# Kernel optimization log

Measured on AMD Instinct MI355X. Metric: run time of the kernel, lower is better.

Reference implementation:

```python
import jax, jax.numpy as jnp
import numpy as np

N, C, H, W = 64, 160, 64, 64
DIM, M = 160, 6
N_ITERS = 2
EPS_LN = 1e-5


def layer_norm(x, g, b):
    mu = jnp.mean(x, axis=-1, keepdims=True)
    var = jnp.var(x, axis=-1, keepdims=True)
    return (x - mu) * jax.lax.rsqrt(var + EPS_LN) * g + b


def setup_inputs() -> dict:
    key = jax.random.key(0)
    ks = jax.random.split(key, 10)
    d = DIM
    lin = lambda k, i, o: jax.random.normal(k, (i, o), jnp.float32) * (1.0 / np.sqrt(i))
    return {
        "feat": jax.random.normal(ks[0], (N, C, H, W), jnp.float32),
        "slots_init": jax.random.normal(ks[1], (M, d), jnp.float32) * 0.02,
        "log_tau": jnp.zeros((1,), jnp.float32),
        "kv_g": jnp.ones((C,), jnp.float32), "kv_b": jnp.zeros((C,), jnp.float32),
        "Wk": lin(ks[2], C, d), "Wv": lin(ks[3], C, d),
        "q_g": jnp.ones((d,), jnp.float32), "q_b": jnp.zeros((d,), jnp.float32),
        "Wq": lin(ks[4], d, d),
        "out_g": jnp.ones((d,), jnp.float32), "out_b": jnp.zeros((d,), jnp.float32),
        "W1": lin(ks[5], d, 2 * d), "b1": jnp.zeros((2 * d,), jnp.float32),
        "W2": lin(ks[6], 2 * d, d), "b2": jnp.zeros((d,), jnp.float32),
    }


def reference(feat, slots_init, log_tau, kv_g, kv_b, Wk, Wv, q_g, q_b, Wq,
              out_g, out_b, W1, b1, W2, b2):
    n, c, h, w = feat.shape
    scale = DIM ** (-0.5)
    # [n, l, c] tokens
    kv_in = layer_norm(feat.reshape(n, c, h * w).transpose(0, 2, 1), kv_g, kv_b)
    k = kv_in @ Wk  # [n, l, d]
    v = kv_in @ Wv  # [n, l, d]
    slots = jnp.broadcast_to(slots_init[None], (n, M, DIM))
    tau = jax.nn.softplus(log_tau) + 0.5  # [1]
    attn = None
    for _ in range(N_ITERS):
        q = layer_norm(slots, q_g, q_b) @ Wq  # [n, m, d]
        logits = jnp.einsum('nmd,nld->nml', q, k) * (scale / tau)
        attn = jax.nn.softmax(logits, axis=1)  # compete over slots
        weights = attn / jnp.clip(attn.sum(axis=-1, keepdims=True), 1e-6)
        updates = jnp.einsum('nml,nld->nmd', weights, v)
        slots = layer_norm(slots + updates, out_g, out_b)
        slots = slots + (jax.nn.gelu(slots @ W1 + b1, approximate=False) @ W2 + b2)
    attn_map = (attn / jnp.clip(attn.sum(axis=-1, keepdims=True), 1e-6)).reshape(n, M, h, w)
    return slots, attn_map
```

## Files before the change

### kernel.cpp

```cpp
#include <hip/hip_runtime.h>
#include <math.h>

#define NN 64
#define CC 160
#define LL 4096
#define DD 160
#define MM 6
#define NCH 64
#define XSTR 68
#define PSPL 8

#if defined(__has_builtin)
#if __has_builtin(__builtin_amdgcn_fdot2_f32_bf16)
#define HAVE_DOT2 1
#endif
#endif

__device__ __forceinline__ unsigned short f2bf(float f) {
  union { float f; unsigned int i; } v; v.f = f;
  unsigned int r = v.i + 0x7fffu + ((v.i >> 16) & 1u);
  return (unsigned short)(r >> 16);
}
__device__ __forceinline__ float u2f_lo(unsigned int w) {
  union { unsigned int i; float f; } v; v.i = w << 16; return v.f;
}
__device__ __forceinline__ float u2f_hi(unsigned int w) {
  union { unsigned int i; float f; } v; v.i = w & 0xffff0000u; return v.f;
}

#if HAVE_DOT2
typedef __bf16 v2bf __attribute__((ext_vector_type(2)));
__device__ __forceinline__ float dot2bf(unsigned int a, unsigned int b, float c) {
  union { unsigned int u; v2bf v; } ua, ub;
  ua.u = a; ub.u = b;
  return __builtin_amdgcn_fdot2_f32_bf16(ua.v, ub.v, c, false);
}
#else
__device__ __forceinline__ float dot2bf(unsigned int a, unsigned int b, float c) {
  return fmaf(u2f_hi(a), u2f_hi(b), fmaf(u2f_lo(a), u2f_lo(b), c));
}
#endif

__global__ __launch_bounds__(256) void k_init(
    const float* log_tau, const float* slots_init, const float* q_g, const float* q_b,
    const float* Wq, const float* Wk, float* Wkq1, float* scal) {
  __shared__ float ln[MM * DD];
  __shared__ float qv[MM * DD];
  __shared__ float mu_s[MM], rs_s[MM];
  int tid = threadIdx.x;
  float x = log_tau[0];
  float sp = (x > 20.f) ? x : log1pf(expf(x));
  float scv = (1.0f / sqrtf((float)DD)) / (sp + 0.5f);
  if (blockIdx.x == 0 && tid == 0) scal[0] = scv;
  if (tid < MM) {
    float s = 0.f, ss = 0.f;
    for (int i = 0; i < DD; i++) { float v = slots_init[tid * DD + i]; s += v; ss += v * v; }
    float mu = s / DD, var = ss / DD - mu * mu;
    mu_s[tid] = mu; rs_s[tid] = rsqrtf(var + 1e-5f);
  }
  __syncthreads();
  for (int o = tid; o < MM * DD; o += 256) {
    int m = o / DD, d = o % DD;
    ln[o] = (slots_init[o] - mu_s[m]) * rs_s[m] * q_g[d] + q_b[d];
  }
  __syncthreads();
  for (int o = tid; o < MM * DD; o += 256) {
    int m = o / DD, d = o % DD;
    float acc = 0.f;
#pragma unroll 8
    for (int i = 0; i < DD; i++) acc += ln[m * DD + i] * Wq[i * DD + d];
    qv[o] = acc;
  }
  __syncthreads();
  for (int o = tid; o < 60; o += 256) {
    int c = blockIdx.x * 10 + o / 6, m = o % 6;
    float acc = 0.f;
#pragma unroll 8
    for (int d = 0; d < DD; d++) acc += Wk[c * DD + d] * qv[m * DD + d];
    Wkq1[c * 6 + m] = scv * acc;
  }
}

__global__ __launch_bounds__(256) void k_init2(
    const float* Wkq1, const float* kv_g, const float* kv_b, float* P1, float* ab) {
  int tid = threadIdx.x;
  for (int o = tid; o < DD * 6; o += 256) {
    int c = o / 6;
    P1[o] = kv_g[c] * Wkq1[o];
  }
  if (tid < 192) {
    int grp = tid >> 4;
    int l = tid & 15;
    int m = grp % 6;
    const float* coef = (grp < 6) ? kv_g : kv_b;
    float s = 0.f;
#pragma unroll
    for (int i = 0; i < 10; i++) {
      int c = l + i * 16;
      s += coef[c] * Wkq1[c * 6 + m];
    }
    s += __shfl_xor(s, 1); s += __shfl_xor(s, 2);
    s += __shfl_xor(s, 4); s += __shfl_xor(s, 8);
    if (l == 0) ab[grp] = s;
  }
}

template <bool ITER2>
__global__ __launch_bounds__(256) void k_pass(
    const float* __restrict__ feat, const float* __restrict__ Pg,
    const float* __restrict__ abg, float* __restrict__ Apart,
    float* __restrict__ SWpart, float* __restrict__ attn_out) {
  int b = blockIdx.x;
  int n = b >> 6, ch = b & 63;
  int tid = threadIdx.x;
  int lane = tid & 63, g = tid >> 6;
  int cg = lane >> 4, tl = lane & 15;

  __shared__ __align__(16) unsigned short xb[160 * XSTR];
  __shared__ __align__(8) float part[4][16][4][10];
  __shared__ __align__(16) unsigned int w2_s[32][8];
  __shared__ __align__(16) float P_s[160][8];

  const float* wsrc = ITER2 ? (Pg + (size_t)n * DD * 6) : Pg;
  for (int o = tid; o < DD * 6; o += 256) P_s[o / 6][o % 6] = wsrc[o];
  const float* absrc = ITER2 ? (abg + n * 12) : abg;
  float alpha[6], beta[6];
#pragma unroll
  for (int m = 0; m < 6; m++) { alpha[m] = absrc[m]; beta[m] = absrc[6 + m]; }
  __syncthreads();

  const float* fb = feat + ((size_t)(n * CC + g * 40 + cg)) * LL + ch * 64 + 4 * tl;
  float s4[4] = {0, 0, 0, 0}, ss4[4] = {0, 0, 0, 0};
  float lgr[6][4];
#pragma unroll
  for (int m = 0; m < 6; m++) { lgr[m][0] = 0.f; lgr[m][1] = 0.f; lgr[m][2] = 0.f; lgr[m][3] = 0.f; }
#pragma unroll
  for (int r = 0; r < 10; r++) {
    int c = g * 40 + r * 4 + cg;
    float4 xv = *(const float4*)(fb + (size_t)(r * 4) * LL);
    float4 p03 = *(const float4*)&P_s[c][0];
    float2 p45 = *(const float2*)&P_s[c][4];
    float xs[4] = {xv.x, xv.y, xv.z, xv.w};
#pragma unroll
    for (int j = 0; j < 4; j++) {
      float x = xs[j];
      s4[j] += x; ss4[j] = fmaf(x, x, ss4[j]);
      lgr[0][j] = fmaf(x, p03.x, lgr[0][j]); lgr[1][j] = fmaf(x, p03.y, lgr[1][j]);
      lgr[2][j] = fmaf(x, p03.z, lgr[2][j]); lgr[3][j] = fmaf(x, p03.w, lgr[3][j]);
      lgr[4][j] = fmaf(x, p45.x, lgr[4][j]); lgr[5][j] = fmaf(x, p45.y, lgr[5][j]);
    }
    uint2 pk;
    pk.x = (unsigned int)f2bf(xv.x) | ((unsigned int)f2bf(xv.y) << 16);
    pk.y = (unsigned int)f2bf(xv.z) | ((unsigned int)f2bf(xv.w) << 16);
    *(uint2*)&xb[c * XSTR + 4 * tl] = pk;
  }
#pragma unroll
  for (int j = 0; j < 4; j++) {
    s4[j] += __shfl_xor(s4[j], 16);  s4[j] += __shfl_xor(s4[j], 32);
    ss4[j] += __shfl_xor(ss4[j], 16); ss4[j] += __shfl_xor(ss4[j], 32);
#pragma unroll
    for (int m = 0; m < 6; m++) {
      lgr[m][j] += __shfl_xor(lgr[m][j], 16);
      lgr[m][j] += __shfl_xor(lgr[m][j], 32);
    }
  }
  if (cg == 0) {
#pragma unroll
    for (int j = 0; j < 4; j++) {
      float* pp = &part[g][tl][j][0];
      *(float2*)&pp[0] = make_float2(s4[j], ss4[j]);
      *(float2*)&pp[2] = make_float2(lgr[0][j], lgr[1][j]);
      *(float2*)&pp[4] = make_float2(lgr[2][j], lgr[3][j]);
      *(float2*)&pp[6] = make_float2(lgr[4][j], lgr[5][j]);
    }
  }
  __syncthreads();

  {
    int tg = lane >> 2, tj = lane & 3;
    float S = 0.f, SS = 0.f, L[6] = {0, 0, 0, 0, 0, 0};
#pragma unroll
    for (int g2 = 0; g2 < 4; g2++) {
      const float* pp = &part[g2][tg][tj][0];
      float2 a = *(const float2*)&pp[0];
      float2 b2_ = *(const float2*)&pp[2];
      float2 c2 = *(const float2*)&pp[4];
      float2 d2 = *(const float2*)&pp[6];
      S += a.x; SS += a.y;
      L[0] += b2_.x; L[1] += b2_.y; L[2] += c2.x; L[3] += c2.y; L[4] += d2.x; L[5] += d2.y;
    }
    float mu = S * (1.0f / CC);
    float var = SS * (1.0f / CC) - mu * mu;
    float rs = rsqrtf(var + 1e-5f);
    float lg[6];
#pragma unroll
    for (int m = 0; m < 6; m++) lg[m] = rs * L[m] - rs * mu * alpha[m] + beta[m];
    float mx = lg[0];
#pragma unroll
    for (int m = 1; m < 6; m++) mx = fmaxf(mx, lg[m]);
    float e[6], sum = 0.f;
#pragma unroll
    for (int m = 0; m < 6; m++) { e[m] = __expf(lg[m] - mx); sum += e[m]; }
    float inv = 1.0f / sum;
    float att[6], wv[6];
#pragma unroll
    for (int m = 0; m < 6; m++) { att[m] = e[m] * inv; wv[m] = att[m] * rs; }

    if (g == 0) {
      float wo[6];
#pragma unroll
      for (int m = 0; m < 6; m++) wo[m] = __shfl_xor(wv[m], 1);
      if (!(lane & 1)) {
        int tp = lane >> 1;
        unsigned int pk[6];
#pragma unroll
        for (int m = 0; m < 6; m++) pk[m] = (unsigned int)f2bf(wv[m]) | ((unsigned int)f2bf(wo[m]) << 16);
        *(uint4*)&w2_s[tp][0] = make_uint4(pk[0], pk[1], pk[2], pk[3]);
        *(uint2*)&w2_s[tp][4] = make_uint2(pk[4], pk[5]);
      }
    } else if (g == 1) {
      if (ITER2) {
        size_t ob = ((size_t)(n * MM)) * LL + ch * 64 + lane;
#pragma unroll
        for (int m = 0; m < 6; m++) attn_out[ob + (size_t)m * LL] = att[m];
      }
    } else if (g == 2) {
#pragma unroll
      for (int m = 0; m < 6; m++) {
        float v = att[m];
        v += __shfl_xor(v, 1);  v += __shfl_xor(v, 2);  v += __shfl_xor(v, 4);
        v += __shfl_xor(v, 8);  v += __shfl_xor(v, 16); v += __shfl_xor(v, 32);
        if (lane == 0) SWpart[b * 12 + m] = v;
      }
    } else {
#pragma unroll
      for (int m = 0; m < 6; m++) {
        float v = wv[m] * mu;
        v += __shfl_xor(v, 1);  v += __shfl_xor(v, 2);  v += __shfl_xor(v, 4);
        v += __shfl_xor(v, 8);  v += __shfl_xor(v, 16); v += __shfl_xor(v, 32);
        if (lane == 0) SWpart[b * 12 + 6 + m] = v;
      }
    }
  }
  __syncthreads();

  if (tid < DD) {
    float A0 = 0.f, A1 = 0.f, A2 = 0.f, A3 = 0.f, A4 = 0.f, A5 = 0.f;
    const unsigned short* xr = &xb[tid * XSTR];
#pragma unroll
    for (int k = 0; k < 16; k++) {
      uint2 xw = *(const uint2*)(xr + 4 * k);
      uint4 wa0 = *(const uint4*)&w2_s[2 * k][0];
      uint2 wb0 = *(const uint2*)&w2_s[2 * k][4];
      uint4 wa1 = *(const uint4*)&w2_s[2 * k + 1][0];
      uint2 wb1 = *(const uint2*)&w2_s[2 * k + 1][4];
      A0 = dot2bf(wa0.x, xw.x, A0); A1 = dot2bf(wa0.y, xw.x, A1);
      A2 = dot2bf(wa0.z, xw.x, A2); A3 = dot2bf(wa0.w, xw.x, A3);
      A4 = dot2bf(wb0.x, xw.x, A4); A5 = dot2bf(wb0.y, xw.x, A5);
      A0 = dot2bf(wa1.x, xw.y, A0); A1 = dot2bf(wa1.y, xw.y, A1);
      A2 = dot2bf(wa1.z, xw.y, A2); A3 = dot2bf(wa1.w, xw.y, A3);
      A4 = dot2bf(wb1.x, xw.y, A4); A5 = dot2bf(wb1.y, xw.y, A5);
    }
    float Aacc[6] = {A0, A1, A2, A3, A4, A5};
#pragma unroll
    for (int m = 0; m < 6; m++) Apart[((size_t)b * 6 + m) * DD + tid] = Aacc[m];
  }
}

__global__ __launch_bounds__(256) void k_reduce(
    const float* __restrict__ Apart, const float* __restrict__ SWpart,
    float* __restrict__ Ared8, float* __restrict__ SWred8) {
  int b = blockIdx.x;
  int n = b / 48;
  int r = b % 48;
  int m = r >> 3, ps = r & 7;
  int tid = threadIdx.x;
  if (tid < DD) {
    const float* src = Apart + ((size_t)(n * NCH + ps * 8) * 6 + m) * DD + tid;
    float s0 = src[0 * 6 * DD] + src[1 * 6 * DD];
    float s1 = src[2 * 6 * DD] + src[3 * 6 * DD];
    float s2 = src[4 * 6 * DD] + src[5 * 6 * DD];
    float s3 = src[6 * 6 * DD] + src[7 * 6 * DD];
    Ared8[((size_t)(n * PSPL + ps) * 6 + m) * DD + tid] = (s0 + s1) + (s2 + s3);
  } else if (m == 0 && tid >= 192 && tid < 204) {
    int k = tid - 192;
    const float* src = SWpart + (size_t)(n * NCH + ps * 8) * 12 + k;
    float s0 = src[0 * 12] + src[1 * 12];
    float s1 = src[2 * 12] + src[3 * 12];
    float s2 = src[4 * 12] + src[5 * 12];
    float s3 = src[6 * 12] + src[7 * 12];
    SWred8[(n * PSPL + ps) * 12 + k] = (s0 + s1) + (s2 + s3);
  }
}

template <bool FIRST, bool LAST>
__global__ __launch_bounds__(256) void k_slot3(
    const float* __restrict__ slots_init, const float* __restrict__ Ared8,
    const float* __restrict__ SWred8, const float* __restrict__ Wv,
    const float* __restrict__ out_g, const float* __restrict__ out_b,
    const float* __restrict__ W1, const float* __restrict__ b1,
    const float* __restrict__ W2, const float* __restrict__ b2,
    const float* __restrict__ q_g, const float* __restrict__ q_b,
    const float* __restrict__ Wq, const float* __restrict__ Wk,
    const float* __restrict__ kv_g, const float* __restrict__ kv_b,
    const float* __restrict__ scal,
    float* __restrict__ slotbuf, float* __restrict__ P2, float* __restrict__ ab2,
    float* __restrict__ Sfin, float* __restrict__ out_slots) {
  int b = blockIdx.x;
  int n = b / MM, m = b % MM;
  int tid = threadIdx.x;
  __shared__ float a_s[DD];
  __shared__ float s1[DD];
  __shared__ float h[320];
  __shared__ float pg[DD], pb[DD];
  __shared__ float sw_s[2];
  __shared__ float Sv_s, mu_s, rs_s;

  if (tid < 16) {
    int ps = tid & 7, which = tid >> 3;
    float v = SWred8[(size_t)(n * PSPL + ps) * 12 + m + 6 * which];
    v += __shfl_xor(v, 1); v += __shfl_xor(v, 2); v += __shfl_xor(v, 4);
    if (ps == 0) {
      if (which == 0) {
        sw_s[0] = v;
        float sc = fmaxf(v, 1e-6f);
        Sv_s = sc;
        if (LAST) Sfin[n * 6 + m] = sc;
      } else {
        sw_s[1] = v;
      }
    }
  }
  __syncthreads();
  if (tid < DD) {
    const float* src = Ared8 + ((size_t)(n * PSPL) * 6 + m) * DD + tid;
    float ar = 0.f;
#pragma unroll
    for (int ps = 0; ps < PSPL; ps++) ar += src[(size_t)ps * 6 * DD];
    a_s[tid] = kv_g[tid] * (ar - sw_s[1]) + kv_b[tid] * sw_s[0];
  }
  __syncthreads();
  if (tid < DD) {
    float u = 0.f;
#pragma unroll 8
    for (int c = 0; c < DD; c++) u = fmaf(a_s[c], Wv[c * DD + tid], u);
    float prev = FIRST ? slots_init[m * DD + tid] : slotbuf[(size_t)n * MM * DD + m * DD + tid];
    s1[tid] = prev + u / Sv_s;
  }
  __syncthreads();
  if (tid < 64) {
    float x0 = s1[tid], x1 = s1[tid + 64], x2 = (tid < 32) ? s1[tid + 128] : 0.f;
    float s = x0 + x1 + x2, ss = x0 * x0 + x1 * x1 + x2 * x2;
#pragma unroll
    for (int off = 32; off >= 1; off >>= 1) { s += __shfl_xor(s, off); ss += __shfl_xor(ss, off); }
    if (tid == 0) {
      float mu = s / DD, var = ss / DD - mu * mu;
      mu_s = mu; rs_s = rsqrtf(var + 1e-5f);
    }
  }
  __syncthreads();
  if (tid < DD) s1[tid] = (s1[tid] - mu_s) * rs_s * out_g[tid] + out_b[tid];
  __syncthreads();
  for (int j = tid; j < 320; j += 256) {
    float acc = b1[j];
#pragma unroll 8
    for (int d = 0; d < DD; d++) acc = fmaf(s1[d], W1[d * 320 + j], acc);
    h[j] = 0.5f * acc * (1.0f + erff(acc * 0.70710678118f));
  }
  __syncthreads();
  if (tid < DD) {
    float acc = b2[tid];
#pragma unroll 8
    for (int j = 0; j < 320; j++) acc = fmaf(h[j], W2[j * DD + tid], acc);
    float val = s1[tid] + acc;
    a_s[tid] = val;
    if (LAST) out_slots[(size_t)n * MM * DD + m * DD + tid] = val;
    else slotbuf[(size_t)n * MM * DD + m * DD + tid] = val;
  }
  if (!LAST) {
    __syncthreads();
    if (tid < 64) {
      float x0 = a_s[tid], x1 = a_s[tid + 64], x2 = (tid < 32) ? a_s[tid + 128] : 0.f;
      float s = x0 + x1 + x2, ss = x0 * x0 + x1 * x1 + x2 * x2;
#pragma unroll
      for (int off = 32; off >= 1; off >>= 1) { s += __shfl_xor(s, off); ss += __shfl_xor(ss, off); }
      if (tid == 0) {
        float mu = s / DD, var = ss / DD - mu * mu;
        mu_s = mu; rs_s = rsqrtf(var + 1e-5f);
      }
    }
    __syncthreads();
    if (tid < DD) s1[tid] = (a_s[tid] - mu_s) * rs_s * q_g[tid] + q_b[tid];
    __syncthreads();
    if (tid < DD) {
      float acc = 0.f;
#pragma unroll 8
      for (int i = 0; i < DD; i++) acc = fmaf(s1[i], Wq[i * DD + tid], acc);
      h[tid] = acc;
    }
    __syncthreads();
    {
      int grp = tid >> 4, l = tid & 15;
      float sc = scal[0];
#pragma unroll 2
      for (int p = 0; p < 10; p++) {
        int c = p * 16 + grp;
        float s = 0.f;
#pragma unroll
        for (int i = 0; i < 10; i++) {
          int d = l + i * 16;
          s = fmaf(Wk[c * DD + d], h[d], s);
        }
        s += __shfl_xor(s, 1); s += __shfl_xor(s, 2);
        s += __shfl_xor(s, 4); s += __shfl_xor(s, 8);
        if (l == 0) {
          float wr = sc * s;
          float gv = kv_g[c] * wr;
          P2[(size_t)n * DD * 6 + c * 6 + m] = gv;
          pg[c] = gv;
          pb[c] = kv_b[c] * wr;
        }
      }
    }
    __syncthreads();
    if (tid < 128) {
      int w = tid >> 6, l = tid & 63;
      const float* src = (w == 0) ? pg : pb;
      float x0 = src[l], x1 = src[l + 64], x2 = (l < 32) ? src[l + 128] : 0.f;
      float s = x0 + x1 + x2;
#pragma unroll
      for (int off = 32; off >= 1; off >>= 1) s += __shfl_xor(s, off);
      if (l == 0) ab2[n * 12 + 6 * w + m] = s;
    }
  }
}

__global__ __launch_bounds__(256) void k_norm(float* attn, const float* Sfin) {
  int idx = blockIdx.x * 256 + threadIdx.x;
  size_t base = (size_t)idx * 4;
  int nm = (int)(base >> 12);
  float s = Sfin[nm];
  float4 v = *(float4*)(attn + base);
  float inv = 1.0f / s;
  v.x *= inv; v.y *= inv; v.z *= inv; v.w *= inv;
  *(float4*)(attn + base) = v;
}

extern "C" void kernel_launch(void* const* d_in, const int* in_sizes, int n_in,
                              void* d_out, int out_size, void* d_ws, size_t ws_size,
                              hipStream_t stream) {
  const float* feat       = (const float*)d_in[0];
  const float* slots_init = (const float*)d_in[1];
  const float* log_tau    = (const float*)d_in[2];
  const float* kv_g       = (const float*)d_in[3];
  const float* kv_b       = (const float*)d_in[4];
  const float* Wk         = (const float*)d_in[5];
  const float* Wv         = (const float*)d_in[6];
  const float* q_g        = (const float*)d_in[7];
  const float* q_b        = (const float*)d_in[8];
  const float* Wq         = (const float*)d_in[9];
  const float* out_g      = (const float*)d_in[10];
  const float* out_b      = (const float*)d_in[11];
  const float* W1         = (const float*)d_in[12];
  const float* b1         = (const float*)d_in[13];
  const float* W2         = (const float*)d_in[14];
  const float* b2         = (const float*)d_in[15];
  float* out = (float*)d_out;
  float* out_attn = out + NN * MM * DD;

  float* Wkq1   = (float*)d_ws;
  float* ab     = Wkq1 + DD * 6;
  float* P1     = ab + 16;
  float* P2     = P1 + DD * 6;
  float* ab2    = P2 + (size_t)NN * DD * 6;
  float* Apart  = ab2 + NN * 12;
  float* SWpart = Apart + (size_t)NN * NCH * MM * DD;
  float* Ared8  = SWpart + (size_t)NN * NCH * 12;
  float* SWred8 = Ared8 + (size_t)NN * PSPL * MM * DD;
  float* Sfin   = SWred8 + NN * PSPL * 12;
  float* scal   = Sfin + NN * MM;
  float* slotbuf = scal + 8;
  size_t required = (size_t)((char*)(slotbuf + NN * MM * DD) - (char*)d_ws);
  if (ws_size < required) return;

  k_init<<<16, 256, 0, stream>>>(log_tau, slots_init, q_g, q_b, Wq, Wk, Wkq1, scal);
  k_init2<<<1, 256, 0, stream>>>(Wkq1, kv_g, kv_b, P1, ab);
  k_pass<false><<<NN * NCH, 256, 0, stream>>>(feat, P1, ab, Apart, SWpart, out_attn);
  k_reduce<<<NN * MM * PSPL, 256, 0, stream>>>(Apart, SWpart, Ared8, SWred8);
  k_slot3<true, false><<<NN * MM, 256, 0, stream>>>(slots_init, Ared8, SWred8, Wv, out_g, out_b,
                                                    W1, b1, W2, b2, q_g, q_b, Wq, Wk, kv_g, kv_b, scal,
                                                    slotbuf, P2, ab2, Sfin, out);
  k_pass<true><<<NN * NCH, 256, 0, stream>>>(feat, P2, ab2, Apart, SWpart, out_attn);
  k_reduce<<<NN * MM * PSPL, 256, 0, stream>>>(Apart, SWpart, Ared8, SWred8);
  k_slot3<false, true><<<NN * MM, 256, 0, stream>>>(slots_init, Ared8, SWred8, Wv, out_g, out_b,
                                                    W1, b1, W2, b2, q_g, q_b, Wq, Wk, kv_g, kv_b, scal,
                                                    slotbuf, P2, ab2, Sfin, out);
  k_norm<<<(NN * MM * LL) / 1024, 256, 0, stream>>>(out_attn, Sfin);
}
```

Baseline: 223.8 us.

## Process four token tiles per pass block and drop separate reduce kernel

Each k_pass block now loops over four 64-token tiles, accumulating the slot-update partials and softmax sums in registers across tiles. This cuts the block count from 64 to 16 per image. Per-block partials shrink enough that k_slot3 reads the 16 partials directly, so the k_reduce launches and their global round trip are removed. In exchange there are fewer blocks, which may lower parallelism on a large GPU, and an extra barrier per tile inside each block.

```diff
diff --git a/kernel.cpp b/kernel.cpp
--- a/kernel.cpp
+++ b/kernel.cpp
@@ -6,9 +6,9 @@
 #define LL 4096
 #define DD 160
 #define MM 6
-#define NCH 64
+#define NCH 16
+#define NT 4
 #define XSTR 68
-#define PSPL 8
 
 #if defined(__has_builtin)
 #if __has_builtin(__builtin_amdgcn_fdot2_f32_bf16)
@@ -111,7 +111,7 @@
     const float* __restrict__ abg, float* __restrict__ Apart,
     float* __restrict__ SWpart, float* __restrict__ attn_out) {
   int b = blockIdx.x;
-  int n = b >> 6, ch = b & 63;
+  int n = b >> 4, ch = b & 15;
   int tid = threadIdx.x;
   int lane = tid & 63, g = tid >> 6;
   int cg = lane >> 4, tl = lane & 15;
@@ -127,176 +127,158 @@
   float alpha[6], beta[6];
 #pragma unroll
   for (int m = 0; m < 6; m++) { alpha[m] = absrc[m]; beta[m] = absrc[6 + m]; }
-  __syncthreads();
-
-  const float* fb = feat + ((size_t)(n * CC + g * 40 + cg)) * LL + ch * 64 + 4 * tl;
-  float s4[4] = {0, 0, 0, 0}, ss4[4] = {0, 0, 0, 0};
-  float lgr[6][4];
-#pragma unroll
-  for (int m = 0; m < 6; m++) { lgr[m][0] = 0.f; lgr[m][1] = 0.f; lgr[m][2] = 0.f; lgr[m][3] = 0.f; }
-#pragma unroll
-  for (int r = 0; r < 10; r++) {
-    int c = g * 40 + r * 4 + cg;
-    float4 xv = *(const float4*)(fb + (size_t)(r * 4) * LL);
-    float4 p03 = *(const float4*)&P_s[c][0];
-    float2 p45 = *(const float2*)&P_s[c][4];
-    float xs[4] = {xv.x, xv.y, xv.z, xv.w};
+  float Aacc[6] = {0, 0, 0, 0, 0, 0};
+  float Sacc[6] = {0, 0, 0, 0, 0, 0};
+  __syncthreads();
+
+  const float* fb0 = feat + ((size_t)(n * CC + g * 40 + cg)) * LL + ch * (64 * NT) + 4 * tl;
+
+#pragma unroll 1
+  for (int t4 = 0; t4 < NT; t4++) {
+    const float* fb = fb0 + t4 * 64;
+    float s4[4] = {0, 0, 0, 0}, ss4[4] = {0, 0, 0, 0};
+    float lgr[6][4];
+#pragma unroll
+    for (int m = 0; m < 6; m++) { lgr[m][0] = 0.f; lgr[m][1] = 0.f; lgr[m][2] = 0.f; lgr[m][3] = 0.f; }
+#pragma unroll
+    for (int r = 0; r < 10; r++) {
+      int c = g * 40 + r * 4 + cg;
+      float4 xv = *(const float4*)(fb + (size_t)(r * 4) * LL);
+      float4 p03 = *(const float4*)&P_s[c][0];
+      float2 p45 = *(const float2*)&P_s[c][4];
+      float xs[4] = {xv.x, xv.y, xv.z, xv.w};
+#pragma unroll
+      for (int j = 0; j < 4; j++) {
+        float x = xs[j];
+        s4[j] += x; ss4[j] = fmaf(x, x, ss4[j]);
+        lgr[0][j] = fmaf(x, p03.x, lgr[0][j]); lgr[1][j] = fmaf(x, p03.y, lgr[1][j]);
+        lgr[2][j] = fmaf(x, p03.z, lgr[2][j]); lgr[3][j] = fmaf(x, p03.w, lgr[3][j]);
+        lgr[4][j] = fmaf(x, p45.x, lgr[4][j]); lgr[5][j] = fmaf(x, p45.y, lgr[5][j]);
+      }
+      uint2 pk;
+      pk.x = (unsigned int)f2bf(xv.x) | ((unsigned int)f2bf(xv.y) << 16);
+      pk.y = (unsigned int)f2bf(xv.z) | ((unsigned int)f2bf(xv.w) << 16);
+      *(uint2*)&xb[c * XSTR + 4 * tl] = pk;
+    }
 #pragma unroll
     for (int j = 0; j < 4; j++) {
-      float x = xs[j];
-      s4[j] += x; ss4[j] = fmaf(x, x, ss4[j]);
-      lgr[0][j] = fmaf(x, p03.x, lgr[0][j]); lgr[1][j] = fmaf(x, p03.y, lgr[1][j]);
-      lgr[2][j] = fmaf(x, p03.z, lgr[2][j]); lgr[3][j] = fmaf(x, p03.w, lgr[3][j]);
-      lgr[4][j] = fmaf(x, p45.x, lgr[4][j]); lgr[5][j] = fmaf(x, p45.y, lgr[5][j]);
-    }
-    uint2 pk;
-    pk.x = (unsigned int)f2bf(xv.x) | ((unsigned int)f2bf(xv.y) << 16);
-    pk.y = (unsigned int)f2bf(xv.z) | ((unsigned int)f2bf(xv.w) << 16);
-    *(uint2*)&xb[c * XSTR + 4 * tl] = pk;
-  }
-#pragma unroll
-  for (int j = 0; j < 4; j++) {
-    s4[j] += __shfl_xor(s4[j], 16);  s4[j] += __shfl_xor(s4[j], 32);
-    ss4[j] += __shfl_xor(ss4[j], 16); ss4[j] += __shfl_xor(ss4[j], 32);
+      s4[j] += __shfl_xor(s4[j], 16);  s4[j] += __shfl_xor(s4[j], 32);
+      ss4[j] += __shfl_xor(ss4[j], 16); ss4[j] += __shfl_xor(ss4[j], 32);
+#pragma unroll
+      for (int m = 0; m < 6; m++) {
+        lgr[m][j] += __shfl_xor(lgr[m][j], 16);
+        lgr[m][j] += __shfl_xor(lgr[m][j], 32);
+      }
+    }
+    if (cg == 0) {
+#pragma unroll
+      for (int j = 0; j < 4; j++) {
+        float* pp = &part[g][tl][j][0];
+        *(float2*)&pp[0] = make_float2(s4[j], ss4[j]);
+        *(float2*)&pp[2] = make_float2(lgr[0][j], lgr[1][j]);
+        *(float2*)&pp[4] = make_float2(lgr[2][j], lgr[3][j]);
+        *(float2*)&pp[6] = make_float2(lgr[4][j], lgr[5][j]);
+      }
+    }
+    __syncthreads();
+
+    {
+      int tg = lane >> 2, tj = lane & 3;
+      float S = 0.f, SS = 0.f, L[6] = {0, 0, 0, 0, 0, 0};
+#pragma unroll
+      for (int g2 = 0; g2 < 4; g2++) {
+        const float* pp = &part[g2][tg][tj][0];
+        float2 a = *(const float2*)&pp[0];
+        float2 b2_ = *(const float2*)&pp[2];
+        float2 c2 = *(const float2*)&pp[4];
+        float2 d2 = *(const float2*)&pp[6];
+        S += a.x; SS += a.y;
+        L[0] += b2_.x; L[1] += b2_.y; L[2] += c2.x; L[3] += c2.y; L[4] += d2.x; L[5] += d2.y;
+      }
+      float mu = S * (1.0f / CC);
+      float var = SS * (1.0f / CC) - mu * mu;
+      float rs = rsqrtf(var + 1e-5f);
+      float lg[6];
+#pragma unroll
+      for (int m = 0; m < 6; m++) lg[m] = rs * L[m] - rs * mu * alpha[m] + beta[m];
+      float mx = lg[0];
+#pragma unroll
+      for (int m = 1; m < 6; m++) mx = fmaxf(mx, lg[m]);
+      float e[6], sum = 0.f;
+#pragma unroll
+      for (int m = 0; m < 6; m++) { e[m] = __expf(lg[m] - mx); sum += e[m]; }
+      float inv = 1.0f / sum;
+      float att[6], wv[6];
+#pragma unroll
+      for (int m = 0; m < 6; m++) { att[m] = e[m] * inv; wv[m] = att[m] * rs; }
+
+      if (g == 0) {
+        float wo[6];
+#pragma unroll
+        for (int m = 0; m < 6; m++) wo[m] = __shfl_xor(wv[m], 1);
+        if (!(lane & 1)) {
+          int tp = lane >> 1;
+          unsigned int pk[6];
+#pragma unroll
+          for (int m = 0; m < 6; m++) pk[m] = (unsigned int)f2bf(wv[m]) | ((unsigned int)f2bf(wo[m]) << 16);
+          *(uint4*)&w2_s[tp][0] = make_uint4(pk[0], pk[1], pk[2], pk[3]);
+          *(uint2*)&w2_s[tp][4] = make_uint2(pk[4], pk[5]);
+        }
+      } else if (g == 1) {
+        if (ITER2) {
+          size_t ob = ((size_t)(n * MM)) * LL + ch * (64 * NT) + t4 * 64 + lane;
+#pragma unroll
+          for (int m = 0; m < 6; m++) attn_out[ob + (size_t)m * LL] = att[m];
+        }
+      } else if (g == 2) {
+#pragma unroll
+        for (int m = 0; m < 6; m++) Sacc[m] += att[m];
+      } else {
+#pragma unroll
+        for (int m = 0; m < 6; m++) Sacc[m] += wv[m] * mu;
+      }
+    }
+    __syncthreads();
+
+    if (tid < DD) {
+      const unsigned short* xr = &xb[tid * XSTR];
+#pragma unroll
+      for (int k = 0; k < 16; k++) {
+        uint2 xw = *(const uint2*)(xr + 4 * k);
+        uint4 wa0 = *(const uint4*)&w2_s[2 * k][0];
+        uint2 wb0 = *(const uint2*)&w2_s[2 * k][4];
+        uint4 wa1 = *(const uint4*)&w2_s[2 * k + 1][0];
+        uint2 wb1 = *(const uint2*)&w2_s[2 * k + 1][4];
+        Aacc[0] = dot2bf(wa0.x, xw.x, Aacc[0]); Aacc[1] = dot2bf(wa0.y, xw.x, Aacc[1]);
+        Aacc[2] = dot2bf(wa0.z, xw.x, Aacc[2]); Aacc[3] = dot2bf(wa0.w, xw.x, Aacc[3]);
+        Aacc[4] = dot2bf(wb0.x, xw.x, Aacc[4]); Aacc[5] = dot2bf(wb0.y, xw.x, Aacc[5]);
+        Aacc[0] = dot2bf(wa1.x, xw.y, Aacc[0]); Aacc[1] = dot2bf(wa1.y, xw.y, Aacc[1]);
+        Aacc[2] = dot2bf(wa1.z, xw.y, Aacc[2]); Aacc[3] = dot2bf(wa1.w, xw.y, Aacc[3]);
+        Aacc[4] = dot2bf(wb1.x, xw.y, Aacc[4]); Aacc[5] = dot2bf(wb1.y, xw.y, Aacc[5]);
+      }
+    }
+    __syncthreads();
+  }
+
+  if (g == 2 || g == 3) {
 #pragma unroll
     for (int m = 0; m < 6; m++) {
-      lgr[m][j] += __shfl_xor(lgr[m][j], 16);
-      lgr[m][j] += __shfl_xor(lgr[m][j], 32);
-    }
-  }
-  if (cg == 0) {
-#pragma unroll
-    for (int j = 0; j < 4; j++) {
-      float* pp = &part[g][tl][j][0];
-      *(float2*)&pp[0] = make_float2(s4[j], ss4[j]);
-      *(float2*)&pp[2] = make_float2(lgr[0][j], lgr[1][j]);
-      *(float2*)&pp[4] = make_float2(lgr[2][j], lgr[3][j]);
-      *(float2*)&pp[6] = make_float2(lgr[4][j], lgr[5][j]);
-    }
-  }
-  __syncthreads();
-
-  {
-    int tg = lane >> 2, tj = lane & 3;
-    float S = 0.f, SS = 0.f, L[6] = {0, 0, 0, 0, 0, 0};
-#pragma unroll
-    for (int g2 = 0; g2 < 4; g2++) {
-      const float* pp = &part[g2][tg][tj][0];
-      float2 a = *(const float2*)&pp[0];
-      float2 b2_ = *(const float2*)&pp[2];
-      float2 c2 = *(const float2*)&pp[4];
-      float2 d2 = *(const float2*)&pp[6];
-      S += a.x; SS += a.y;
-      L[0] += b2_.x; L[1] += b2_.y; L[2] += c2.x; L[3] += c2.y; L[4] += d2.x; L[5] += d2.y;
-    }
-    float mu = S * (1.0f / CC);
-    float var = SS * (1.0f / CC) - mu * mu;
-    float rs = rsqrtf(var + 1e-5f);
-    float lg[6];
-#pragma unroll
-    for (int m = 0; m < 6; m++) lg[m] = rs * L[m] - rs * mu * alpha[m] + beta[m];
-    float mx = lg[0];
-#pragma unroll
-    for (int m = 1; m < 6; m++) mx = fmaxf(mx, lg[m]);
-    float e[6], sum = 0.f;
-#pragma unroll
-    for (int m = 0; m < 6; m++) { e[m] = __expf(lg[m] - mx); sum += e[m]; }
-    float inv = 1.0f / sum;
-    float att[6], wv[6];
-#pragma unroll
-    for (int m = 0; m < 6; m++) { att[m] = e[m] * inv; wv[m] = att[m] * rs; }
-
-    if (g == 0) {
-      float wo[6];
-#pragma unroll
-      for (int m = 0; m < 6; m++) wo[m] = __shfl_xor(wv[m], 1);
-      if (!(lane & 1)) {
-        int tp = lane >> 1;
-        unsigned int pk[6];
-#pragma unroll
-        for (int m = 0; m < 6; m++) pk[m] = (unsigned int)f2bf(wv[m]) | ((unsigned int)f2bf(wo[m]) << 16);
-        *(uint4*)&w2_s[tp][0] = make_uint4(pk[0], pk[1], pk[2], pk[3]);
-        *(uint2*)&w2_s[tp][4] = make_uint2(pk[4], pk[5]);
-      }
-    } else if (g == 1) {
-      if (ITER2) {
-        size_t ob = ((size_t)(n * MM)) * LL + ch * 64 + lane;
-#pragma unroll
-        for (int m = 0; m < 6; m++) attn_out[ob + (size_t)m * LL] = att[m];
-      }
-    } else if (g == 2) {
-#pragma unroll
-      for (int m = 0; m < 6; m++) {
-        float v = att[m];
-        v += __shfl_xor(v, 1);  v += __shfl_xor(v, 2);  v += __shfl_xor(v, 4);
-        v += __shfl_xor(v, 8);  v += __shfl_xor(v, 16); v += __shfl_xor(v, 32);
-        if (lane == 0) SWpart[b * 12 + m] = v;
-      }
-    } else {
-#pragma unroll
-      for (int m = 0; m < 6; m++) {
-        float v = wv[m] * mu;
-        v += __shfl_xor(v, 1);  v += __shfl_xor(v, 2);  v += __shfl_xor(v, 4);
-        v += __shfl_xor(v, 8);  v += __shfl_xor(v, 16); v += __shfl_xor(v, 32);
-        if (lane == 0) SWpart[b * 12 + 6 + m] = v;
-      }
-    }
-  }
-  __syncthreads();
-
+      float v = Sacc[m];
+      v += __shfl_xor(v, 1);  v += __shfl_xor(v, 2);  v += __shfl_xor(v, 4);
+      v += __shfl_xor(v, 8);  v += __shfl_xor(v, 16); v += __shfl_xor(v, 32);
+      if (lane == 0) SWpart[b * 12 + (g - 2) * 6 + m] = v;
+    }
+  }
   if (tid < DD) {
-    float A0 = 0.f, A1 = 0.f, A2 = 0.f, A3 = 0.f, A4 = 0.f, A5 = 0.f;
-    const unsigned short* xr = &xb[tid * XSTR];
-#pragma unroll
-    for (int k = 0; k < 16; k++) {
-      uint2 xw = *(const uint2*)(xr + 4 * k);
-      uint4 wa0 = *(const uint4*)&w2_s[2 * k][0];
-      uint2 wb0 = *(const uint2*)&w2_s[2 * k][4];
-      uint4 wa1 = *(const uint4*)&w2_s[2 * k + 1][0];
-      uint2 wb1 = *(const uint2*)&w2_s[2 * k + 1][4];
-      A0 = dot2bf(wa0.x, xw.x, A0); A1 = dot2bf(wa0.y, xw.x, A1);
-      A2 = dot2bf(wa0.z, xw.x, A2); A3 = dot2bf(wa0.w, xw.x, A3);
-      A4 = dot2bf(wb0.x, xw.x, A4); A5 = dot2bf(wb0.y, xw.x, A5);
-      A0 = dot2bf(wa1.x, xw.y, A0); A1 = dot2bf(wa1.y, xw.y, A1);
-      A2 = dot2bf(wa1.z, xw.y, A2); A3 = dot2bf(wa1.w, xw.y, A3);
-      A4 = dot2bf(wb1.x, xw.y, A4); A5 = dot2bf(wb1.y, xw.y, A5);
-    }
-    float Aacc[6] = {A0, A1, A2, A3, A4, A5};
 #pragma unroll
     for (int m = 0; m < 6; m++) Apart[((size_t)b * 6 + m) * DD + tid] = Aacc[m];
-  }
-}
-
-__global__ __launch_bounds__(256) void k_reduce(
-    const float* __restrict__ Apart, const float* __restrict__ SWpart,
-    float* __restrict__ Ared8, float* __restrict__ SWred8) {
-  int b = blockIdx.x;
-  int n = b / 48;
-  int r = b % 48;
-  int m = r >> 3, ps = r & 7;
-  int tid = threadIdx.x;
-  if (tid < DD) {
-    const float* src = Apart + ((size_t)(n * NCH + ps * 8) * 6 + m) * DD + tid;
-    float s0 = src[0 * 6 * DD] + src[1 * 6 * DD];
-    float s1 = src[2 * 6 * DD] + src[3 * 6 * DD];
-    float s2 = src[4 * 6 * DD] + src[5 * 6 * DD];
-    float s3 = src[6 * 6 * DD] + src[7 * 6 * DD];
-    Ared8[((size_t)(n * PSPL + ps) * 6 + m) * DD + tid] = (s0 + s1) + (s2 + s3);
-  } else if (m == 0 && tid >= 192 && tid < 204) {
-    int k = tid - 192;
-    const float* src = SWpart + (size_t)(n * NCH + ps * 8) * 12 + k;
-    float s0 = src[0 * 12] + src[1 * 12];
-    float s1 = src[2 * 12] + src[3 * 12];
-    float s2 = src[4 * 12] + src[5 * 12];
-    float s3 = src[6 * 12] + src[7 * 12];
-    SWred8[(n * PSPL + ps) * 12 + k] = (s0 + s1) + (s2 + s3);
   }
 }
 
 template <bool FIRST, bool LAST>
 __global__ __launch_bounds__(256) void k_slot3(
-    const float* __restrict__ slots_init, const float* __restrict__ Ared8,
-    const float* __restrict__ SWred8, const float* __restrict__ Wv,
+    const float* __restrict__ slots_init, const float* __restrict__ Apart,
+    const float* __restrict__ SWpart, const float* __restrict__ Wv,
     const float* __restrict__ out_g, const float* __restrict__ out_b,
     const float* __restrict__ W1, const float* __restrict__ b1,
     const float* __restrict__ W2, const float* __restrict__ b2,
@@ -316,27 +298,26 @@
   __shared__ float sw_s[2];
   __shared__ float Sv_s, mu_s, rs_s;
 
-  if (tid < 16) {
-    int ps = tid & 7, which = tid >> 3;
-    float v = SWred8[(size_t)(n * PSPL + ps) * 12 + m + 6 * which];
-    v += __shfl_xor(v, 1); v += __shfl_xor(v, 2); v += __shfl_xor(v, 4);
-    if (ps == 0) {
+  if (tid < 32) {
+    int p = tid & 15, which = tid >> 4;
+    float v = SWpart[(size_t)(n * NCH + p) * 12 + m + 6 * which];
+    v += __shfl_xor(v, 1); v += __shfl_xor(v, 2);
+    v += __shfl_xor(v, 4); v += __shfl_xor(v, 8);
+    if (p == 0) {
+      sw_s[which] = v;
       if (which == 0) {
-        sw_s[0] = v;
         float sc = fmaxf(v, 1e-6f);
         Sv_s = sc;
         if (LAST) Sfin[n * 6 + m] = sc;
-      } else {
-        sw_s[1] = v;
       }
     }
   }
   __syncthreads();
   if (tid < DD) {
-    const float* src = Ared8 + ((size_t)(n * PSPL) * 6 + m) * DD + tid;
+    const float* src = Apart + ((size_t)(n * NCH) * 6 + m) * DD + tid;
     float ar = 0.f;
 #pragma unroll
-    for (int ps = 0; ps < PSPL; ps++) ar += src[(size_t)ps * 6 * DD];
+    for (int p = 0; p < NCH; p++) ar += src[(size_t)p * 6 * DD];
     a_s[tid] = kv_g[tid] * (ar - sw_s[1]) + kv_b[tid] * sw_s[0];
   }
   __syncthreads();
@@ -475,9 +456,7 @@
   float* ab2    = P2 + (size_t)NN * DD * 6;
   float* Apart  = ab2 + NN * 12;
   float* SWpart = Apart + (size_t)NN * NCH * MM * DD;
-  float* Ared8  = SWpart + (size_t)NN * NCH * 12;
-  float* SWred8 = Ared8 + (size_t)NN * PSPL * MM * DD;
-  float* Sfin   = SWred8 + NN * PSPL * 12;
+  float* Sfin   = SWpart + (size_t)NN * NCH * 12;
   float* scal   = Sfin + NN * MM;
   float* slotbuf = scal + 8;
   size_t required = (size_t)((char*)(slotbuf + NN * MM * DD) - (char*)d_ws);
@@ -486,13 +465,11 @@
   k_init<<<16, 256, 0, stream>>>(log_tau, slots_init, q_g, q_b, Wq, Wk, Wkq1, scal);
   k_init2<<<1, 256, 0, stream>>>(Wkq1, kv_g, kv_b, P1, ab);
   k_pass<false><<<NN * NCH, 256, 0, stream>>>(feat, P1, ab, Apart, SWpart, out_attn);
-  k_reduce<<<NN * MM * PSPL, 256, 0, stream>>>(Apart, SWpart, Ared8, SWred8);
-  k_slot3<true, false><<<NN * MM, 256, 0, stream>>>(slots_init, Ared8, SWred8, Wv, out_g, out_b,
+  k_slot3<true, false><<<NN * MM, 256, 0, stream>>>(slots_init, Apart, SWpart, Wv, out_g, out_b,
                                                     W1, b1, W2, b2, q_g, q_b, Wq, Wk, kv_g, kv_b, scal,
                                                     slotbuf, P2, ab2, Sfin, out);
   k_pass<true><<<NN * NCH, 256, 0, stream>>>(feat, P2, ab2, Apart, SWpart, out_attn);
-  k_reduce<<<NN * MM * PSPL, 256, 0, stream>>>(Apart, SWpart, Ared8, SWred8);
-  k_slot3<false, true><<<NN * MM, 256, 0, stream>>>(slots_init, Ared8, SWred8, Wv, out_g, out_b,
+  k_slot3<false, true><<<NN * MM, 256, 0, stream>>>(slots_init, Apart, SWpart, Wv, out_g, out_b,
                                                     W1, b1, W2, b2, q_g, q_b, Wq, Wk, kv_g, kv_b, scal,
                                                     slotbuf, P2, ab2, Sfin, out);
   k_norm<<<(NN * MM * LL) / 1024, 256, 0, stream>>>(out_attn, Sfin);
```

After: 214.0 us. 1.05x faster.
